# Performance work log

Hardware: AMD Instinct MI355X
Metric: run time of the kernel (lower is better)

## Reference

```python
import jax, jax.numpy as jnp
import numpy as np

B, S, D, E = 4096, 32, 512, 512


def setup_inputs() -> dict:
    key = jax.random.key(0)
    kx, kq, kk, kv = jax.random.split(key, 4)
    return {
        "x": jax.random.normal(kx, (B, S * D), dtype=jnp.float32),
        "Q": jax.random.normal(kq, (S, D, E), dtype=jnp.float32),
        "K": jax.random.normal(kk, (S, D, E), dtype=jnp.float32),
        "V": jax.random.normal(kv, (S, D, E), dtype=jnp.float32),
    }


def reference(x, Q, K, V):
    # x: [B, S*D] -> [B, S, D]; per-segment projections via batched einsum
    b = x.shape[0]
    xs = x.reshape(b, S, D)
    q = jnp.einsum("bsd,sde->bse", xs, Q)  # [B, S, E]
    k = jnp.einsum("bsd,sde->bse", xs, K)
    v = jnp.einsum("bsd,sde->bse", xs, V)
    scores = jnp.sum(q * k, axis=-1)  # [B, S]
    # L2-normalize scores across segments (matches torch norm(dim=1))
    weights = scores / jnp.linalg.norm(scores, axis=1, keepdims=True)
    # weighted sum of per-segment value vectors
    y = jnp.einsum("bs,bse->be", weights, v)  # [B, E]
    return y
```

## Files before the change

kernel.cpp:

```cpp
#include <hip/hip_runtime.h>
#include <hip/hip_bf16.h>
#include <math.h>


typedef __attribute__((ext_vector_type(8))) short s8v;
typedef __attribute__((ext_vector_type(4))) float f4v;

#define MFMA_BF16(a, b, c) __builtin_amdgcn_mfma_f32_16x16x32_bf16((a), (b), (c), 0, 0, 0)

constexpr int NB = 4096;
constexpr int NS = 32;
constexpr int ND = 512;
constexpr int NE = 512;
constexpr int SD = NS * ND;

__device__ __forceinline__ short f2bf(float f) {
  union { float f; unsigned u; } v; v.f = f;
  unsigned r = v.u + 0x7fffu + ((v.u >> 16) & 1u);
  return (short)(r >> 16);
}
__device__ __forceinline__ float bf2f(short h) {
  union { unsigned u; float f; } v; v.u = ((unsigned)(unsigned short)h) << 16;
  return v.f;
}
__device__ __forceinline__ s8v cvt8(const float* p) {
  s8v r;
#pragma unroll
  for (int i = 0; i < 8; ++i) r[i] = f2bf(p[i]);
  return r;
}

__device__ __forceinline__ void gload16(const void* g, void* l) {
  __builtin_amdgcn_global_load_lds(
      (const __attribute__((address_space(1))) unsigned int*)g,
      (__attribute__((address_space(3))) unsigned int*)l, 16, 0, 0);
}

__global__ __launch_bounds__(256) void k_castx(const float* __restrict__ x,
                                               short* __restrict__ xb,
                                               float* __restrict__ scores) {
  size_t gtid = (size_t)blockIdx.x * 256 + threadIdx.x;
  if (gtid < (size_t)NB * NS / 4) {
    f4v z = (f4v)0.0f;
    *(f4v*)(scores + gtid * 4) = z;
  }
  size_t i = gtid * 8;
  f4v a = *(const f4v*)(x + i);
  f4v b = *(const f4v*)(x + i + 4);
  s8v o;
#pragma unroll
  for (int u = 0; u < 4; ++u) { o[u] = f2bf(a[u]); o[4 + u] = f2bf(b[u]); }
  *(s8v*)(xb + i) = o;
}

__global__ __launch_bounds__(256) void k_misc(const float* __restrict__ V,
                                              short* __restrict__ Vt,
                                              const float* __restrict__ Kw,
                                              const float* __restrict__ Qw,
                                              short* __restrict__ G) {
  __shared__ __align__(16) char smem[36864];
  int bid = blockIdx.x;
  int tid = threadIdx.x;

  if (bid >= 512) {
    float (*t)[65] = (float(*)[65])smem;
    int t2 = bid - 512;
    int k0 = (t2 & 255) * 64;
    int e0 = (t2 >> 8) * 64;
#pragma unroll
    for (int i = 0; i < 16; ++i) {
      int idx = tid + 256 * i;
      int r = idx >> 6, c = idx & 63;
      t[r][c] = V[(size_t)(k0 + r) * NE + e0 + c];
    }
    __syncthreads();
#pragma unroll
    for (int i = 0; i < 16; ++i) {
      int idx = tid + 256 * i;
      int e = idx >> 6, k = idx & 63;
      Vt[(size_t)(e0 + e) * SD + k0 + k] = f2bf(t[k][e]);
    }
  } else {
    int t3 = bid;
    int s = t3 >> 4;
    int tm = (t3 >> 2) & 3, tn = t3 & 3;
    const float* A = Kw + (size_t)s * ND * NE + (size_t)tm * 128 * NE;
    const float* B = Qw + (size_t)s * ND * NE + (size_t)tn * 128 * NE;
    short* Gs = G + (size_t)s * ND * ND;

    s8v (*lsA)[9] = (s8v(*)[9])smem;
    s8v (*lsB)[9] = (s8v(*)[9])(smem + 18432);

    int lane = tid & 63, wid = tid >> 6;
    int wr = wid >> 1, wc = wid & 1;
    int lhi = lane >> 4, llo = lane & 15;

    float ra[4][8], rb[4][8];
    f4v acc[4][4];
#pragma unroll
    for (int i = 0; i < 4; ++i)
#pragma unroll
      for (int j = 0; j < 4; ++j) acc[i][j] = (f4v)0.0f;

    auto loadRegs = [&](int k0) {
#pragma unroll
      for (int i = 0; i < 4; ++i) {
        int c = tid + 256 * i; int row = c >> 3, k8 = c & 7;
        const float* p = A + (size_t)row * NE + k0 + k8 * 8;
        *(f4v*)&ra[i][0] = *(const f4v*)p;
        *(f4v*)&ra[i][4] = *(const f4v*)(p + 4);
        const float* q = B + (size_t)row * NE + k0 + k8 * 8;
        *(f4v*)&rb[i][0] = *(const f4v*)q;
        *(f4v*)&rb[i][4] = *(const f4v*)(q + 4);
      }
    };
    auto writeLds = [&]() {
#pragma unroll
      for (int i = 0; i < 4; ++i) {
        int c = tid + 256 * i; int row = c >> 3, k8 = c & 7;
        lsA[row][k8] = cvt8(ra[i]);
        lsB[row][k8] = cvt8(rb[i]);
      }
    };

    loadRegs(0);
    writeLds();
    for (int kt = 0; kt < 8; ++kt) {
      __syncthreads();
      if (kt + 1 < 8) loadRegs((kt + 1) * 64);
#pragma unroll
      for (int kk = 0; kk < 2; ++kk) {
        s8v af[4], bq[4];
#pragma unroll
        for (int i = 0; i < 4; ++i) af[i] = lsA[wr * 64 + i * 16 + llo][kk * 4 + lhi];
#pragma unroll
        for (int j = 0; j < 4; ++j) bq[j] = lsB[wc * 64 + j * 16 + llo][kk * 4 + lhi];
#pragma unroll
        for (int i = 0; i < 4; ++i)
#pragma unroll
          for (int j = 0; j < 4; ++j) acc[i][j] = MFMA_BF16(af[i], bq[j], acc[i][j]);
      }
      __syncthreads();
      if (kt + 1 < 8) writeLds();
    }

#pragma unroll
    for (int i = 0; i < 4; ++i)
#pragma unroll
      for (int r = 0; r < 4; ++r) {
        int row = tm * 128 + wr * 64 + i * 16 + lhi * 4 + r;
#pragma unroll
        for (int j = 0; j < 4; ++j) {
          int col = tn * 128 + wc * 64 + j * 16 + llo;
          Gs[(size_t)row * ND + col] = f2bf(acc[i][j][r]);
        }
      }
  }
}

__global__ __launch_bounds__(256) void k_symm(const short* __restrict__ G,
                                              short* __restrict__ U) {
  int s = blockIdx.y;
  int kt = blockIdx.x >> 3, nt = blockIdx.x & 7;
  const short* Gs = G + (size_t)s * ND * ND;
  short* Us = U + (size_t)s * ND * ND;
  int k0 = kt * 64, n0 = nt * 64;
  int tid = threadIdx.x;
  int r = tid >> 2, cb = (tid & 3) * 16;

  if (kt > nt) {
    s8v z = (s8v)(short)0;
    *(s8v*)&Us[(size_t)(k0 + r) * ND + n0 + cb] = z;
    *(s8v*)&Us[(size_t)(k0 + r) * ND + n0 + cb + 8] = z;
    return;
  }

  __shared__ float tt[64][65];
  {
    const short* src = &Gs[(size_t)(n0 + r) * ND + k0 + cb];
    s8v a = *(const s8v*)src;
    s8v b = *(const s8v*)(src + 8);
#pragma unroll
    for (int u = 0; u < 8; ++u) { tt[r][cb + u] = bf2f(a[u]); tt[r][cb + 8 + u] = bf2f(b[u]); }
  }
  __syncthreads();
  {
    const short* src = &Gs[(size_t)(k0 + r) * ND + n0 + cb];
    s8v a = *(const s8v*)src;
    s8v b = *(const s8v*)(src + 8);
    s8v oa, ob;
#pragma unroll
    for (int u = 0; u < 8; ++u) {
      int k = k0 + r;
      int n1 = n0 + cb + u, n2 = n0 + cb + 8 + u;
      float g1 = bf2f(a[u]), g2 = bf2f(b[u]);
      float v1 = (k < n1) ? (g1 + tt[cb + u][r]) : ((k == n1) ? g1 : 0.f);
      float v2 = (k < n2) ? (g2 + tt[cb + 8 + u][r]) : ((k == n2) ? g2 : 0.f);
      oa[u] = f2bf(v1); ob[u] = f2bf(v2);
    }
    short* dst = &Us[(size_t)(k0 + r) * ND + n0 + cb];
    *(s8v*)dst = oa;
    *(s8v*)(dst + 8) = ob;
  }
}

__global__ __launch_bounds__(512, 4) void k_scores(const short* __restrict__ xb,
                                                   const short* __restrict__ U,
                                                   float* __restrict__ scores) {
  int t = blockIdx.x;
  int swz = (t & 7) * 256 + (t >> 3);
  int s = swz >> 6;
  int mt = (swz >> 2) & 15;
  int nt = swz & 3;
  int b0 = mt * 256, n0 = nt * 128;
  const short* Asrc = xb + (size_t)b0 * SD + s * ND;
  const short* Bt = U + (size_t)s * ND * ND + (size_t)n0 * ND;

  __shared__ __align__(16) short lsA[256 * 64];
  __shared__ __align__(16) short lsB[128 * 64];

  int tid = threadIdx.x;
  int lane = tid & 63, wid = tid >> 6;
  int wr = wid >> 1, wc = wid & 1;
  int lhi = lane >> 4, llo = lane & 15;
  int lrow = lane >> 3;
  int scol = ((lane & 7) ^ lrow) * 8;

  f4v acc[4][4];
#pragma unroll
  for (int i = 0; i < 4; ++i)
#pragma unroll
    for (int j = 0; j < 4; ++j) acc[i][j] = (f4v)0.0f;

  for (int kt = 2 * nt; kt < 8; ++kt) {
    int k0 = kt * 64;
#pragma unroll
    for (int c = 0; c < 4; ++c) {
      int chunk = wid * 4 + c;
      int row = chunk * 8 + lrow;
      gload16(Asrc + (size_t)row * SD + k0 + scol, (char*)lsA + chunk * 1024);
    }
#pragma unroll
    for (int c = 0; c < 2; ++c) {
      int chunk = wid * 2 + c;
      int row = chunk * 8 + lrow;
      gload16(Bt + (size_t)row * ND + k0 + scol, (char*)lsB + chunk * 1024);
    }
    __syncthreads();
    const s8v* fA = (const s8v*)lsA;
    const s8v* fB = (const s8v*)lsB;
#pragma unroll
    for (int kk = 0; kk < 2; ++kk) {
      s8v af[4], bq[4];
      int cc = kk * 4 + lhi;
      int ccs = cc ^ (llo & 7);
#pragma unroll
      for (int i = 0; i < 4; ++i) af[i] = fA[(wr * 64 + i * 16 + llo) * 8 + ccs];
#pragma unroll
      for (int j = 0; j < 4; ++j) bq[j] = fB[(wc * 64 + j * 16 + llo) * 8 + ccs];
#pragma unroll
      for (int i = 0; i < 4; ++i)
#pragma unroll
        for (int j = 0; j < 4; ++j) acc[i][j] = MFMA_BF16(af[i], bq[j], acc[i][j]);
    }
    __syncthreads();
  }

#pragma unroll
  for (int i = 0; i < 4; ++i)
#pragma unroll
    for (int r = 0; r < 4; ++r) {
      int rowl = wr * 64 + i * 16 + lhi * 4 + r;
      int b = b0 + rowl;
      const short* xr = xb + (size_t)b * SD + s * ND + n0 + wc * 64;
      float v = 0.f;
#pragma unroll
      for (int j = 0; j < 4; ++j) v += bf2f(xr[j * 16 + llo]) * acc[i][j][r];
      v += __shfl_xor(v, 1);
      v += __shfl_xor(v, 2);
      v += __shfl_xor(v, 4);
      v += __shfl_xor(v, 8);
      if (llo == 0) atomicAdd(&scores[b * NS + s], v);
    }
}

__global__ __launch_bounds__(256) void k_weights(const float* __restrict__ scores,
                                                 float* __restrict__ w) {
  int b = blockIdx.x * 256 + threadIdx.x;
  float sq = 0.f, sc[NS];
#pragma unroll
  for (int s = 0; s < NS; ++s) { sc[s] = scores[b * NS + s]; sq += sc[s] * sc[s]; }
  float inv = 1.0f / sqrtf(sq);
#pragma unroll
  for (int s = 0; s < NS; ++s) w[b * NS + s] = sc[s] * inv;
}

__global__ __launch_bounds__(256, 4) void k_out(const short* __restrict__ xb,
                                                const float* __restrict__ wts,
                                                const short* __restrict__ Vt,
                                                short* __restrict__ y_part) {
  int t = blockIdx.x;
  int kg = t & 7;
  int nt = (t >> 3) & 1;
  int mt = t >> 4;
  int b0 = mt * 64, n0 = nt * 256;
  const short* Asrc = xb + (size_t)b0 * SD + kg * 2048;
  const short* Bsrc = Vt + (size_t)n0 * SD + kg * 2048;
  short* yp = y_part + (size_t)kg * NB * NE;

  __shared__ __align__(16) short lsA[64 * 64];
  __shared__ __align__(16) short lsB[256 * 64];

  int tid = threadIdx.x;
  int lane = tid & 63, wid = tid >> 6;
  int lhi = lane >> 4, llo = lane & 15;
  int lrow = lane >> 3;
  int scol = ((lane & 7) ^ lrow) * 8;

  int arow0 = tid >> 3;
  int arow1 = 32 + (tid >> 3);
  int acb = (tid & 7) * 8;
  int awoff = (arow0 * 8 + ((tid & 7) ^ (arow0 & 7))) * 16;

  f4v acc[4][4];
#pragma unroll
  for (int i = 0; i < 4; ++i)
#pragma unroll
    for (int j = 0; j < 4; ++j) acc[i][j] = (f4v)0.0f;

  for (int sl = 0; sl < 4; ++sl) {
    int s = kg * 4 + sl;
    float w0 = wts[(b0 + arow0) * NS + s];
    float w1 = wts[(b0 + arow1) * NS + s];
#pragma unroll 1
    for (int k8 = 0; k8 < 8; ++k8) {
      int k0 = sl * 512 + k8 * 64;
#pragma unroll
      for (int c = 0; c < 8; ++c) {
        int chunk = wid * 8 + c;
        int row = chunk * 8 + lrow;
        gload16(Bsrc + (size_t)row * SD + k0 + scol, (char*)lsB + chunk * 1024);
      }
      s8v a0 = *(const s8v*)(Asrc + (size_t)arow0 * SD + k0 + acb);
      s8v a1 = *(const s8v*)(Asrc + (size_t)arow1 * SD + k0 + acb);
      s8v o0, o1;
#pragma unroll
      for (int u = 0; u < 8; ++u) {
        o0[u] = f2bf(bf2f(a0[u]) * w0);
        o1[u] = f2bf(bf2f(a1[u]) * w1);
      }
      *(s8v*)((char*)lsA + awoff) = o0;
      *(s8v*)((char*)lsA + 4096 + awoff) = o1;
      __syncthreads();
      const s8v* fA = (const s8v*)lsA;
      const s8v* fB = (const s8v*)lsB;
#pragma unroll
      for (int kk = 0; kk < 2; ++kk) {
        s8v af[4], bq[4];
        int cc = kk * 4 + lhi;
        int ccs = cc ^ (llo & 7);
#pragma unroll
        for (int i = 0; i < 4; ++i) af[i] = fA[(i * 16 + llo) * 8 + ccs];
#pragma unroll
        for (int j = 0; j < 4; ++j) bq[j] = fB[(wid * 64 + j * 16 + llo) * 8 + ccs];
#pragma unroll
        for (int i = 0; i < 4; ++i)
#pragma unroll
          for (int j = 0; j < 4; ++j) acc[i][j] = MFMA_BF16(af[i], bq[j], acc[i][j]);
      }
      __syncthreads();
    }
  }

#pragma unroll
  for (int i = 0; i < 4; ++i)
#pragma unroll
    for (int r = 0; r < 4; ++r) {
      int row = b0 + i * 16 + lhi * 4 + r;
#pragma unroll
      for (int j = 0; j < 4; ++j) {
        int col = n0 + wid * 64 + j * 16 + llo;
        yp[(size_t)row * NE + col] = f2bf(acc[i][j][r]);
      }
    }
}

__global__ __launch_bounds__(256) void k_reduce(const short* __restrict__ y_part,
                                                float* __restrict__ y) {
  size_t f = ((size_t)blockIdx.x * 256 + threadIdx.x) * 8;
  float acc[8];
#pragma unroll
  for (int u = 0; u < 8; ++u) acc[u] = 0.f;
#pragma unroll
  for (int kg = 0; kg < 8; ++kg) {
    s8v v = *(const s8v*)(y_part + (size_t)kg * NB * NE + f);
#pragma unroll
    for (int u = 0; u < 8; ++u) acc[u] += bf2f(v[u]);
  }
  *(f4v*)(y + f) = *(f4v*)&acc[0];
  *(f4v*)(y + f + 4) = *(f4v*)&acc[4];
}

extern "C" void kernel_launch(void* const* d_in, const int* in_sizes, int n_in,
                              void* d_out, int out_size, void* d_ws, size_t ws_size,
                              hipStream_t stream) {
  const float* x  = (const float*)d_in[0];
  const float* Qw = (const float*)d_in[1];
  const float* Kw = (const float*)d_in[2];
  const float* Vw = (const float*)d_in[3];
  float* y = (float*)d_out;

  char* ws = (char*)d_ws;
  short* xb     = (short*)ws;
  short* G      = (short*)(ws + (size_t)128 * 1024 * 1024);
  short* Vt     = (short*)(ws + (size_t)144 * 1024 * 1024);
  short* Ut     = (short*)(ws + (size_t)160 * 1024 * 1024);
  float* scores = (float*)(ws + (size_t)176 * 1024 * 1024);
  float* wts    = (float*)(ws + (size_t)176 * 1024 * 1024 + 512 * 1024);
  short* y_part = (short*)(ws + (size_t)192 * 1024 * 1024);

  k_castx<<<32768, 256, 0, stream>>>(x, xb, scores);
  k_misc<<<2560, 256, 0, stream>>>(Vw, Vt, Kw, Qw, G);
  k_symm<<<dim3(64, NS), 256, 0, stream>>>(G, Ut);
  k_scores<<<2048, 512, 0, stream>>>(xb, Ut, scores);
  k_weights<<<16, 256, 0, stream>>>(scores, wts);
  k_out<<<1024, 256, 0, stream>>>(xb, wts, Vt, y_part);
  k_reduce<<<1024, 256, 0, stream>>>(y_part, y);
}
```

Before: 318.6 us.

## Merge cast and prep kernels; vectorize V transpose stores; halve GEMM K-tile

Folds the x-to-bf16 cast and score zeroing into the weight-prep kernel as extra blocks, removing one launch and letting the cast overlap with the Gram GEMM and V transpose. The V transpose now writes 16-byte vectors per thread instead of scalar shorts. The K^T Q GEMM tile shrinks its K step from 64 to 32, cutting LDS from about 36KB to about 16KB to allow more resident blocks, at the cost of twice as many barrier-separated iterations. The LDS row layout loses its padding, which may introduce bank conflicts.

```diff
diff --git a/kernel.cpp b/kernel.cpp
--- a/kernel.cpp
+++ b/kernel.cpp
@@ -36,33 +36,32 @@
       (__attribute__((address_space(3))) unsigned int*)l, 16, 0, 0);
 }
 
-__global__ __launch_bounds__(256) void k_castx(const float* __restrict__ x,
+__global__ __launch_bounds__(256) void k_prep2(const float* __restrict__ x,
                                                short* __restrict__ xb,
-                                               float* __restrict__ scores) {
-  size_t gtid = (size_t)blockIdx.x * 256 + threadIdx.x;
-  if (gtid < (size_t)NB * NS / 4) {
-    f4v z = (f4v)0.0f;
-    *(f4v*)(scores + gtid * 4) = z;
-  }
-  size_t i = gtid * 8;
-  f4v a = *(const f4v*)(x + i);
-  f4v b = *(const f4v*)(x + i + 4);
-  s8v o;
-#pragma unroll
-  for (int u = 0; u < 4; ++u) { o[u] = f2bf(a[u]); o[4 + u] = f2bf(b[u]); }
-  *(s8v*)(xb + i) = o;
-}
-
-__global__ __launch_bounds__(256) void k_misc(const float* __restrict__ V,
-                                              short* __restrict__ Vt,
-                                              const float* __restrict__ Kw,
-                                              const float* __restrict__ Qw,
-                                              short* __restrict__ G) {
-  __shared__ __align__(16) char smem[36864];
+                                               float* __restrict__ scores,
+                                               const float* __restrict__ V,
+                                               short* __restrict__ Vt,
+                                               const float* __restrict__ Kw,
+                                               const float* __restrict__ Qw,
+                                               short* __restrict__ G) {
+  __shared__ __align__(16) char smem[16640];
   int bid = blockIdx.x;
   int tid = threadIdx.x;
 
-  if (bid >= 512) {
+  if (bid >= 2560) {
+    size_t gtid = (size_t)(bid - 2560) * 256 + tid;
+    if (gtid < (size_t)NB * NS / 4) {
+      f4v z = (f4v)0.0f;
+      *(f4v*)(scores + gtid * 4) = z;
+    }
+    size_t i = gtid * 8;
+    f4v a = *(const f4v*)(x + i);
+    f4v b = *(const f4v*)(x + i + 4);
+    s8v o;
+#pragma unroll
+    for (int u = 0; u < 4; ++u) { o[u] = f2bf(a[u]); o[4 + u] = f2bf(b[u]); }
+    *(s8v*)(xb + i) = o;
+  } else if (bid >= 512) {
     float (*t)[65] = (float(*)[65])smem;
     int t2 = bid - 512;
     int k0 = (t2 & 255) * 64;
@@ -74,28 +73,32 @@
       t[r][c] = V[(size_t)(k0 + r) * NE + e0 + c];
     }
     __syncthreads();
-#pragma unroll
-    for (int i = 0; i < 16; ++i) {
-      int idx = tid + 256 * i;
-      int e = idx >> 6, k = idx & 63;
-      Vt[(size_t)(e0 + e) * SD + k0 + k] = f2bf(t[k][e]);
-    }
+    int e = tid >> 2, kb = (tid & 3) * 16;
+    s8v o1, o2;
+#pragma unroll
+    for (int u = 0; u < 8; ++u) {
+      o1[u] = f2bf(t[kb + u][e]);
+      o2[u] = f2bf(t[kb + 8 + u][e]);
+    }
+    short* dst = Vt + (size_t)(e0 + e) * SD + k0 + kb;
+    *(s8v*)dst = o1;
+    *(s8v*)(dst + 8) = o2;
   } else {
-    int t3 = bid;
-    int s = t3 >> 4;
-    int tm = (t3 >> 2) & 3, tn = t3 & 3;
+    int s = bid >> 4;
+    int tm = (bid >> 2) & 3, tn = bid & 3;
     const float* A = Kw + (size_t)s * ND * NE + (size_t)tm * 128 * NE;
     const float* B = Qw + (size_t)s * ND * NE + (size_t)tn * 128 * NE;
     short* Gs = G + (size_t)s * ND * ND;
 
-    s8v (*lsA)[9] = (s8v(*)[9])smem;
-    s8v (*lsB)[9] = (s8v(*)[9])(smem + 18432);
+    s8v (*lsA)[4] = (s8v(*)[4])smem;
+    s8v (*lsB)[4] = (s8v(*)[4])(smem + 8192);
 
     int lane = tid & 63, wid = tid >> 6;
     int wr = wid >> 1, wc = wid & 1;
     int lhi = lane >> 4, llo = lane & 15;
-
-    float ra[4][8], rb[4][8];
+    int srow = tid >> 1, sch = (tid & 1) * 16;
+
+    float ra[16], rb[16];
     f4v acc[4][4];
 #pragma unroll
     for (int i = 0; i < 4; ++i)
@@ -103,45 +106,38 @@
       for (int j = 0; j < 4; ++j) acc[i][j] = (f4v)0.0f;
 
     auto loadRegs = [&](int k0) {
-#pragma unroll
-      for (int i = 0; i < 4; ++i) {
-        int c = tid + 256 * i; int row = c >> 3, k8 = c & 7;
-        const float* p = A + (size_t)row * NE + k0 + k8 * 8;
-        *(f4v*)&ra[i][0] = *(const f4v*)p;
-        *(f4v*)&ra[i][4] = *(const f4v*)(p + 4);
-        const float* q = B + (size_t)row * NE + k0 + k8 * 8;
-        *(f4v*)&rb[i][0] = *(const f4v*)q;
-        *(f4v*)&rb[i][4] = *(const f4v*)(q + 4);
+      const float* p = A + (size_t)srow * NE + k0 + sch;
+      const float* q = B + (size_t)srow * NE + k0 + sch;
+#pragma unroll
+      for (int v = 0; v < 4; ++v) {
+        *(f4v*)&ra[v * 4] = *(const f4v*)(p + v * 4);
+        *(f4v*)&rb[v * 4] = *(const f4v*)(q + v * 4);
       }
     };
     auto writeLds = [&]() {
-#pragma unroll
-      for (int i = 0; i < 4; ++i) {
-        int c = tid + 256 * i; int row = c >> 3, k8 = c & 7;
-        lsA[row][k8] = cvt8(ra[i]);
-        lsB[row][k8] = cvt8(rb[i]);
-      }
+      int cg = (tid & 1) * 2;
+      lsA[srow][cg] = cvt8(ra);
+      lsA[srow][cg + 1] = cvt8(ra + 8);
+      lsB[srow][cg] = cvt8(rb);
+      lsB[srow][cg + 1] = cvt8(rb + 8);
     };
 
     loadRegs(0);
     writeLds();
-    for (int kt = 0; kt < 8; ++kt) {
+    for (int kt = 0; kt < 16; ++kt) {
       __syncthreads();
-      if (kt + 1 < 8) loadRegs((kt + 1) * 64);
-#pragma unroll
-      for (int kk = 0; kk < 2; ++kk) {
-        s8v af[4], bq[4];
-#pragma unroll
-        for (int i = 0; i < 4; ++i) af[i] = lsA[wr * 64 + i * 16 + llo][kk * 4 + lhi];
-#pragma unroll
-        for (int j = 0; j < 4; ++j) bq[j] = lsB[wc * 64 + j * 16 + llo][kk * 4 + lhi];
-#pragma unroll
-        for (int i = 0; i < 4; ++i)
-#pragma unroll
-          for (int j = 0; j < 4; ++j) acc[i][j] = MFMA_BF16(af[i], bq[j], acc[i][j]);
-      }
+      if (kt + 1 < 16) loadRegs((kt + 1) * 32);
+      s8v af[4], bq[4];
+#pragma unroll
+      for (int i = 0; i < 4; ++i) af[i] = lsA[wr * 64 + i * 16 + llo][lhi];
+#pragma unroll
+      for (int j = 0; j < 4; ++j) bq[j] = lsB[wc * 64 + j * 16 + llo][lhi];
+#pragma unroll
+      for (int i = 0; i < 4; ++i)
+#pragma unroll
+        for (int j = 0; j < 4; ++j) acc[i][j] = MFMA_BF16(af[i], bq[j], acc[i][j]);
       __syncthreads();
-      if (kt + 1 < 8) writeLds();
+      if (kt + 1 < 16) writeLds();
     }
 
 #pragma unroll
@@ -419,8 +415,7 @@
   float* wts    = (float*)(ws + (size_t)176 * 1024 * 1024 + 512 * 1024);
   short* y_part = (short*)(ws + (size_t)192 * 1024 * 1024);
 
-  k_castx<<<32768, 256, 0, stream>>>(x, xb, scores);
-  k_misc<<<2560, 256, 0, stream>>>(Vw, Vt, Kw, Qw, G);
+  k_prep2<<<35328, 256, 0, stream>>>(x, xb, scores, Vw, Vt, Kw, Qw, G);
   k_symm<<<dim3(64, NS), 256, 0, stream>>>(G, Ut);
   k_scores<<<2048, 512, 0, stream>>>(xb, Ut, scores);
   k_weights<<<16, 256, 0, stream>>>(scores, wts);
```

Measured after the change: 321.3 us. Within noise of the previous version (+0.8%).
